# Performance work log

Hardware: AMD Instinct MI355X
Metric: run time of the kernel (lower is better)

The kernel has to match this reference:

```python
import jax, jax.numpy as jnp
import numpy as np

EMBED_DIM = 1024
HEAD_DIM = 64


def setup_inputs() -> dict:
    key = jax.random.key(0)
    ks = jax.random.split(key, 7)
    B, S = 4, 2048
    s = 1.0 / np.sqrt(EMBED_DIM)
    h = jax.random.normal(ks[0], (B, S, EMBED_DIM), dtype=jnp.float32)
    Wq = jax.random.normal(ks[1], (EMBED_DIM, HEAD_DIM), dtype=jnp.float32) * s
    bq = jax.random.normal(ks[2], (HEAD_DIM,), dtype=jnp.float32) * 0.01
    Wk = jax.random.normal(ks[3], (EMBED_DIM, HEAD_DIM), dtype=jnp.float32) * s
    bk = jax.random.normal(ks[4], (HEAD_DIM,), dtype=jnp.float32) * 0.01
    Wv = jax.random.normal(ks[5], (EMBED_DIM, HEAD_DIM), dtype=jnp.float32) * s
    bv = jax.random.normal(ks[6], (HEAD_DIM,), dtype=jnp.float32) * 0.01
    return {"h": h, "Wq": Wq, "bq": bq, "Wk": Wk, "bk": bk, "Wv": Wv, "bv": bv}


def reference(h, Wq, bq, Wk, bk, Wv, bv):
    # Linear projections: h [B,S,E] -> q,k [B,S,D]
    q = jnp.einsum("bse,ed->bsd", h, Wq) + bq
    k = jnp.einsum("bse,ed->bsd", h, Wk) + bk
    v = jnp.einsum("bse,ed->bsd", h, Wv) + bv  # computed but UNUSED (faithful to source)
    del v
    scale = 1.0 / jnp.sqrt(jnp.asarray(HEAD_DIM, dtype=q.dtype))
    # scores [B, Sq, Sk]
    scores = jnp.einsum("bqd,bkd->bqk", q, k) * scale
    # NOTE: source uses softmax over dim=1 (query axis), not the key axis
    weights = jax.nn.softmax(scores, axis=1)
    # NOTE: source passes h (not v) as the value tensor
    out = jnp.einsum("bqk,bke->bqe", weights, h)  # [B, Sq, E]
    return out
```

## Files before the change

kernel.cpp:

```cpp
#include <hip/hip_runtime.h>
#include <hip/hip_bf16.h>
#include <math.h>

#define EMBED 1024
#define HDIM  64
#define BATCH 4
#define SEQ   2048

typedef __attribute__((ext_vector_type(8))) short short8;
typedef __attribute__((ext_vector_type(4))) float f32x4;
typedef unsigned int u32;
typedef unsigned short u16;

static __device__ __forceinline__ u16 f2bf(float f) {
    union { float f; u32 u; } v; v.f = f;
    u32 r = v.u + 0x7fffu + ((v.u >> 16) & 1u);
    return (u16)(r >> 16);
}

static __device__ __forceinline__ void gload_lds16(const u16* g, u16* l) {
    __builtin_amdgcn_global_load_lds(
        (const __attribute__((address_space(1))) u32*)g,
        (__attribute__((address_space(3))) u32*)l, 16, 0, 0);
}

__global__ __launch_bounds__(256) void wt_kernel(
    const float* __restrict__ Wq, const float* __restrict__ Wk,
    u16* __restrict__ WqT, u16* __restrict__ WkT)
{
    __shared__ float tile[64][65];
    const float* W = blockIdx.y ? Wk : Wq;
    u16* WT = blockIdx.y ? WkT : WqT;
    int e0 = blockIdx.x * 64;
    int t = threadIdx.x, c = t & 63, r4 = t >> 6;
    for (int r = r4; r < 64; r += 4)
        tile[r][c] = W[(size_t)(e0 + r) * HDIM + c];
    __syncthreads();
    for (int d = r4; d < 64; d += 4)
        WT[(size_t)d * EMBED + e0 + c] = f2bf(tile[c][d]);
}

__global__ __launch_bounds__(256) void proj_kernel(
    const float* __restrict__ h, const u16* __restrict__ WqT, const u16* __restrict__ WkT,
    const float* __restrict__ bq, const float* __restrict__ bk,
    u16* __restrict__ Qbf, u16* __restrict__ Kbf)
{
    __shared__ u16 hs[2][16][136];
    int b = blockIdx.x >> 7, s0 = (blockIdx.x & 127) * 16;
    int t = threadIdx.x, lane = t & 63, w = t >> 6;
    int l15 = lane & 15, quad = lane >> 4;
    int pj = w >> 1, nh = (w & 1) * 32;
    const float* hb = h + ((size_t)b * SEQ + s0) * EMBED;
    const u16* Wp = pj ? WkT : WqT;
    int r = t >> 4, c4 = (t & 15) * 4;

    f32x4 pre0 = *(const f32x4*)(hb + (size_t)r * EMBED + c4);
    f32x4 pre1 = *(const f32x4*)(hb + (size_t)r * EMBED + 64 + c4);
    f32x4 accA[2], accB[2];
    accA[0] = accA[1] = accB[0] = accB[1] = (f32x4){0.f, 0.f, 0.f, 0.f};

    const u16* Wrow0 = Wp + (size_t)(nh + l15) * EMBED;
    const u16* Wrow1 = Wp + (size_t)(nh + 16 + l15) * EMBED;

    short8 cw[8];
#pragma unroll
    for (int i = 0; i < 4; i++) {
        cw[i]     = *(const short8*)(Wrow0 + i * 32 + quad * 8);
        cw[4 + i] = *(const short8*)(Wrow1 + i * 32 + quad * 8);
    }

    for (int it = 0; it < 8; ++it) {
        int ec = it * 128, buf = it & 1;
        uint2 pk;
        pk.x = (u32)f2bf(pre0[0]) | ((u32)f2bf(pre0[1]) << 16);
        pk.y = (u32)f2bf(pre0[2]) | ((u32)f2bf(pre0[3]) << 16);
        *(uint2*)&hs[buf][r][c4] = pk;
        pk.x = (u32)f2bf(pre1[0]) | ((u32)f2bf(pre1[1]) << 16);
        pk.y = (u32)f2bf(pre1[2]) | ((u32)f2bf(pre1[3]) << 16);
        *(uint2*)&hs[buf][r][64 + c4] = pk;
        __syncthreads();

        if (it + 1 < 8) {
            pre0 = *(const f32x4*)(hb + (size_t)r * EMBED + ec + 128 + c4);
            pre1 = *(const f32x4*)(hb + (size_t)r * EMBED + ec + 192 + c4);
        }
        short8 nw[8];
#pragma unroll
        for (int i = 0; i < 8; i++) nw[i] = cw[i];
        if (it + 1 < 8) {
#pragma unroll
            for (int i = 0; i < 4; i++) {
                nw[i]     = *(const short8*)(Wrow0 + ec + 128 + i * 32 + quad * 8);
                nw[4 + i] = *(const short8*)(Wrow1 + ec + 128 + i * 32 + quad * 8);
            }
        }

        short8 a0 = *(const short8*)&hs[buf][l15][quad * 8];
        short8 a1 = *(const short8*)&hs[buf][l15][32 + quad * 8];
        short8 a2 = *(const short8*)&hs[buf][l15][64 + quad * 8];
        short8 a3 = *(const short8*)&hs[buf][l15][96 + quad * 8];
        accA[0] = __builtin_amdgcn_mfma_f32_16x16x32_bf16(a0, cw[0], accA[0], 0, 0, 0);
        accA[1] = __builtin_amdgcn_mfma_f32_16x16x32_bf16(a0, cw[4], accA[1], 0, 0, 0);
        accB[0] = __builtin_amdgcn_mfma_f32_16x16x32_bf16(a1, cw[1], accB[0], 0, 0, 0);
        accB[1] = __builtin_amdgcn_mfma_f32_16x16x32_bf16(a1, cw[5], accB[1], 0, 0, 0);
        accA[0] = __builtin_amdgcn_mfma_f32_16x16x32_bf16(a2, cw[2], accA[0], 0, 0, 0);
        accA[1] = __builtin_amdgcn_mfma_f32_16x16x32_bf16(a2, cw[6], accA[1], 0, 0, 0);
        accB[0] = __builtin_amdgcn_mfma_f32_16x16x32_bf16(a3, cw[3], accB[0], 0, 0, 0);
        accB[1] = __builtin_amdgcn_mfma_f32_16x16x32_bf16(a3, cw[7], accB[1], 0, 0, 0);
#pragma unroll
        for (int i = 0; i < 8; i++) cw[i] = nw[i];
    }

    const float* bias = pj ? bk : bq;
    float scale = pj ? 1.0f : 0.125f;
    u16* outp = pj ? Kbf : Qbf;
    float bv0 = bias[nh + l15], bv1 = bias[nh + 16 + l15];
#pragma unroll
    for (int rr = 0; rr < 4; rr++) {
        size_t row = (size_t)b * SEQ + s0 + quad * 4 + rr;
        outp[row * HDIM + nh + l15]      = f2bf((accA[0][rr] + accB[0][rr] + bv0) * scale);
        outp[row * HDIM + nh + 16 + l15] = f2bf((accA[1][rr] + accB[1][rr] + bv1) * scale);
    }
}

__global__ __launch_bounds__(256) void sw_kernel(
    const u16* __restrict__ Qbf, const u16* __restrict__ Kbf,
    u16* __restrict__ Wmat, float* __restrict__ invl)
{
    __shared__ float sl[4][16];
    int b = blockIdx.y;
    int k0 = blockIdx.x * 16;
    int t = threadIdx.x, lane = t & 63, w = t >> 6;
    int l15 = lane & 15, quad = lane >> 4;
    const u16* Qb = Qbf + (size_t)b * SEQ * HDIM;
    const u16* Kb = Kbf + (size_t)b * SEQ * HDIM;
    u16* Wb = Wmat + (size_t)b * SEQ * SEQ;
    short8 kf0 = *(const short8*)(Kb + (size_t)(k0 + l15) * HDIM + quad * 8);
    short8 kf1 = *(const short8*)(Kb + (size_t)(k0 + l15) * HDIM + 32 + quad * 8);
    f32x4 lacc = {0.f, 0.f, 0.f, 0.f};
    int qs = w * 512;
    const u16* qpa = Qb + (size_t)(qs + l15) * HDIM;
    const u16* qpb = Qb + (size_t)(qs + 16 + l15) * HDIM;
    short8 cf0a = *(const short8*)(qpa + quad * 8);
    short8 cf1a = *(const short8*)(qpa + 32 + quad * 8);
    short8 cf0b = *(const short8*)(qpb + quad * 8);
    short8 cf1b = *(const short8*)(qpb + 32 + quad * 8);

    for (int q0 = qs; q0 < qs + 512; q0 += 32) {
        short8 nf0a = cf0a, nf1a = cf1a, nf0b = cf0b, nf1b = cf1b;
        if (q0 + 32 < qs + 512) {
            const u16* na = Qb + (size_t)(q0 + 32 + l15) * HDIM;
            const u16* nb = Qb + (size_t)(q0 + 48 + l15) * HDIM;
            nf0a = *(const short8*)(na + quad * 8);
            nf1a = *(const short8*)(na + 32 + quad * 8);
            nf0b = *(const short8*)(nb + quad * 8);
            nf1b = *(const short8*)(nb + 32 + quad * 8);
        }
        f32x4 aa = {0.f, 0.f, 0.f, 0.f}, ab = {0.f, 0.f, 0.f, 0.f};
        aa = __builtin_amdgcn_mfma_f32_16x16x32_bf16(kf0, cf0a, aa, 0, 0, 0);
        ab = __builtin_amdgcn_mfma_f32_16x16x32_bf16(kf0, cf0b, ab, 0, 0, 0);
        aa = __builtin_amdgcn_mfma_f32_16x16x32_bf16(kf1, cf1a, aa, 0, 0, 0);
        ab = __builtin_amdgcn_mfma_f32_16x16x32_bf16(kf1, cf1b, ab, 0, 0, 0);
        float e0 = __expf(aa[0]), e1 = __expf(aa[1]);
        float e2 = __expf(aa[2]), e3 = __expf(aa[3]);
        float g0 = __expf(ab[0]), g1 = __expf(ab[1]);
        float g2 = __expf(ab[2]), g3 = __expf(ab[3]);
        lacc[0] += e0 + g0; lacc[1] += e1 + g1;
        lacc[2] += e2 + g2; lacc[3] += e3 + g3;
        uint2 pa, pb;
        pa.x = (u32)f2bf(e0) | ((u32)f2bf(e1) << 16);
        pa.y = (u32)f2bf(e2) | ((u32)f2bf(e3) << 16);
        pb.x = (u32)f2bf(g0) | ((u32)f2bf(g1) << 16);
        pb.y = (u32)f2bf(g2) | ((u32)f2bf(g3) << 16);
        *(uint2*)(Wb + (size_t)(q0 + l15) * SEQ + k0 + quad * 4) = pa;
        *(uint2*)(Wb + (size_t)(q0 + 16 + l15) * SEQ + k0 + quad * 4) = pb;
        cf0a = nf0a; cf1a = nf1a; cf0b = nf0b; cf1b = nf1b;
    }
#pragma unroll
    for (int m = 1; m <= 8; m <<= 1) {
        lacc[0] += __shfl_xor(lacc[0], m, 64);
        lacc[1] += __shfl_xor(lacc[1], m, 64);
        lacc[2] += __shfl_xor(lacc[2], m, 64);
        lacc[3] += __shfl_xor(lacc[3], m, 64);
    }
    if (l15 == 0) {
        sl[w][quad * 4 + 0] = lacc[0];
        sl[w][quad * 4 + 1] = lacc[1];
        sl[w][quad * 4 + 2] = lacc[2];
        sl[w][quad * 4 + 3] = lacc[3];
    }
    __syncthreads();
    if (t < 16)
        invl[b * SEQ + k0 + t] =
            1.0f / ((sl[0][t] + sl[1][t]) + (sl[2][t] + sl[3][t]));
}

__global__ __launch_bounds__(256) void tscale_kernel(
    const float* __restrict__ h, const float* __restrict__ invl,
    u16* __restrict__ hT)
{
    __shared__ float tile[64][65];
    int b  = blockIdx.z;
    int s0 = blockIdx.x * 64, e0 = blockIdx.y * 64;
    int t = threadIdx.x, c = t & 63, r4 = t >> 6;
    const float* hb = h + (size_t)b * SEQ * EMBED;
    for (int r = r4; r < 64; r += 4)
        tile[r][c] = hb[(size_t)(s0 + r) * EMBED + e0 + c];
    __syncthreads();
    float il = invl[b * SEQ + s0 + c];
    u16* hTb = hT + (size_t)b * EMBED * SEQ;
    for (int er = r4; er < 64; er += 4)
        hTb[(size_t)(e0 + er) * SEQ + s0 + c] = f2bf(tile[c][er] * il);
}

__global__ __launch_bounds__(512, 2) void out_gemm_kernel(
    const u16* __restrict__ Wmat, const u16* __restrict__ hT, float* __restrict__ out)
{
    __shared__ u16 As[3][256 * 64];
    __shared__ u16 Bs[3][128 * 64];
    int b = blockIdx.z;
    int q0 = blockIdx.x * 256, e0 = blockIdx.y * 128;
    int t = threadIdx.x, lane = t & 63, w = t >> 6;
    int l15 = lane & 15, quad = lane >> 4;
    const u16* Wb  = Wmat + (size_t)b * SEQ * SEQ;
    const u16* hTb = hT + (size_t)b * EMBED * SEQ;
    int wm = w >> 1, wn = w & 1;
    int wq = wm * 64, we = wn * 64;

    f32x4 acc[4][4];
#pragma unroll
    for (int qi = 0; qi < 4; qi++)
#pragma unroll
        for (int ej = 0; ej < 4; ej++) acc[qi][ej] = (f32x4){0.f, 0.f, 0.f, 0.f};

    int st_rl = lane >> 3;
    int st_pc = lane & 7;

#define STAGE_A(si, k0, ld)                                                    \
    {                                                                          \
        int rowb = w * 32 + (ld) * 8;                                          \
        int row  = rowb + st_rl;                                               \
        int cg   = st_pc ^ (row & 7);                \
        gload_lds16(Wb + (size_t)(q0 + row) * SEQ + (k0) + cg * 8,             \
                    &As[si][rowb * 64] + lane * 8);                            \
    }
#define STAGE_B(si, k0, ld)                                                    \
    {                                                                          \
        int rowb = w * 16 + (ld) * 8;                                          \
        int row  = rowb + st_rl;                                               \
        int cg   = st_pc ^ (row & 7);                                          \
        gload_lds16(hTb + (size_t)(e0 + row) * SEQ + (k0) + cg * 8,            \
                    &Bs[si][rowb * 64] + lane * 8);                            \
    }

#define LDFRAGS(kf)                                                            \
    {                                                                          \
        _Pragma("unroll")                                                      \
        for (int i = 0; i < 4; i++) {                                          \
            int ra  = wq + i * 16 + l15;                                       \
            int pca = ((kf) * 4 + quad) ^ (ra & 7);                            \
            af[i] = *(const short8*)(Ab + ra * 64 + pca * 8);                  \
        }                                                                      \
        _Pragma("unroll")                                                      \
        for (int j = 0; j < 4; j++) {                                          \
            int rb  = we + j * 16 + l15;                                       \
            int pcb = ((kf) * 4 + quad) ^ (rb & 7);                            \
            bfr[j] = *(const short8*)(Bb + rb * 64 + pcb * 8);                 \
        }                                                                      \
    }

#define MFMA16                                                                 \
    {                                                                          \
        _Pragma("unroll")                                                      \
        for (int qi = 0; qi < 4; qi++)                                         \
            _Pragma("unroll")                                                  \
            for (int ej = 0; ej < 4; ej++)                                     \
                acc[qi][ej] = __builtin_amdgcn_mfma_f32_16x16x32_bf16(         \
                    af[qi], bfr[ej], acc[qi][ej], 0, 0, 0);                    \
    }

    STAGE_A(0, 0, 0) STAGE_A(0, 0, 1) STAGE_A(0, 0, 2) STAGE_A(0, 0, 3)
    STAGE_B(0, 0, 0) STAGE_B(0, 0, 1)
    STAGE_A(1, 64, 0) STAGE_A(1, 64, 1) STAGE_A(1, 64, 2) STAGE_A(1, 64, 3)
    STAGE_B(1, 64, 0) STAGE_B(1, 64, 1)
    asm volatile("s_waitcnt vmcnt(6)" ::: "memory");
    __builtin_amdgcn_s_barrier();

    for (int kt = 0; kt < 32; ++kt) {
        int s = kt % 3;
        const u16* Ab = &As[s][0];
        const u16* Bb = &Bs[s][0];
        int s2 = (kt + 2) % 3;
        int k2 = (kt + 2) * 64;
        bool st = (kt + 2) < 32;
        short8 af[4], bfr[4];

        LDFRAGS(0)
        if (st) { STAGE_A(s2, k2, 0) STAGE_A(s2, k2, 1) STAGE_B(s2, k2, 0) }
        __builtin_amdgcn_s_barrier();
        asm volatile("s_waitcnt lgkmcnt(0)" ::: "memory");
        __builtin_amdgcn_sched_barrier(0);
        __builtin_amdgcn_s_setprio(1);
        MFMA16
        __builtin_amdgcn_s_setprio(0);
        __builtin_amdgcn_s_barrier();

        LDFRAGS(1)
        if (st) { STAGE_A(s2, k2, 2) STAGE_A(s2, k2, 3) STAGE_B(s2, k2, 1) }
        __builtin_amdgcn_s_barrier();
        asm volatile("s_waitcnt lgkmcnt(0)" ::: "memory");
        __builtin_amdgcn_sched_barrier(0);
        __builtin_amdgcn_s_setprio(1);
        MFMA16
        __builtin_amdgcn_s_setprio(0);
        if (kt < 30)       { asm volatile("s_waitcnt vmcnt(6)" ::: "memory"); }
        else if (kt == 30) { asm volatile("s_waitcnt vmcnt(0)" ::: "memory"); }
        __builtin_amdgcn_s_barrier();
    }
#undef STAGE_A
#undef STAGE_B
#undef LDFRAGS
#undef MFMA16

    float* outb = out + (size_t)b * SEQ * EMBED;
#pragma unroll
    for (int qi = 0; qi < 4; qi++)
#pragma unroll
        for (int ej = 0; ej < 4; ej++)
#pragma unroll
            for (int r = 0; r < 4; r++)
                outb[(size_t)(q0 + wq + qi * 16 + quad * 4 + r) * EMBED
                     + e0 + we + ej * 16 + l15] = acc[qi][ej][r];
}

extern "C" void kernel_launch(void* const* d_in, const int* in_sizes, int n_in,
                              void* d_out, int out_size, void* d_ws, size_t ws_size,
                              hipStream_t stream) {
    (void)in_sizes; (void)n_in; (void)out_size; (void)ws_size;
    const float* h  = (const float*)d_in[0];
    const float* Wq = (const float*)d_in[1];
    const float* bq = (const float*)d_in[2];
    const float* Wk = (const float*)d_in[3];
    const float* bk = (const float*)d_in[4];
    float* out = (float*)d_out;

    char* ws = (char*)d_ws;
    u16*   Qbf  = (u16*)(ws);
    u16*   Kbf  = (u16*)(ws + (1ull << 20));
    u16*   hT   = (u16*)(ws + (2ull << 20));
    float* invl = (float*)(ws + (18ull << 20));
    u16*   WqT  = (u16*)(ws + (18ull << 20) + (128ull << 10));
    u16*   WkT  = (u16*)(ws + (18ull << 20) + (256ull << 10));
    u16*   Wmat = (u16*)(ws + (19ull << 20));

    hipLaunchKernelGGL(wt_kernel, dim3(16, 2), dim3(256), 0, stream, Wq, Wk, WqT, WkT);
    hipLaunchKernelGGL(proj_kernel, dim3(512), dim3(256), 0, stream,
                       h, WqT, WkT, bq, bk, Qbf, Kbf);
    hipLaunchKernelGGL(sw_kernel, dim3(128, 4), dim3(256), 0, stream,
                       Qbf, Kbf, Wmat, invl);
    hipLaunchKernelGGL(tscale_kernel, dim3(32, 16, 4), dim3(256), 0, stream,
                       h, invl, hT);
    hipLaunchKernelGGL(out_gemm_kernel, dim3(8, 8, 4), dim3(512), 0, stream,
                       Wmat, hT, out);
}
```

Measured before the change: 178.2 us.

## Split K across warp groups in out GEMM, vectorize transpose, deepen proj prefetch

The output GEMM now assigns each group of four warps one half of each 64-wide K slice, so every warp covers a 128x64 output tile with 8x4 accumulators. The two halves are summed through shared memory in the epilogue. This cuts per-warp B-fragment reloads and raises MFMA work per LDS read, at the cost of doubled accumulator registers, which may hurt occupancy at 2 blocks per CU. The transpose-scale kernel switches to float4 loads and packed 4-element bf16 stores. The projection kernel prefetches h two iterations ahead instead of one.

```diff
diff --git a/kernel.cpp b/kernel.cpp
--- a/kernel.cpp
+++ b/kernel.cpp
@@ -54,8 +54,10 @@
     const u16* Wp = pj ? WkT : WqT;
     int r = t >> 4, c4 = (t & 15) * 4;
 
-    f32x4 pre0 = *(const f32x4*)(hb + (size_t)r * EMBED + c4);
-    f32x4 pre1 = *(const f32x4*)(hb + (size_t)r * EMBED + 64 + c4);
+    f32x4 preA0 = *(const f32x4*)(hb + (size_t)r * EMBED + c4);
+    f32x4 preA1 = *(const f32x4*)(hb + (size_t)r * EMBED + 64 + c4);
+    f32x4 preB0 = *(const f32x4*)(hb + (size_t)r * EMBED + 128 + c4);
+    f32x4 preB1 = *(const f32x4*)(hb + (size_t)r * EMBED + 192 + c4);
     f32x4 accA[2], accB[2];
     accA[0] = accA[1] = accB[0] = accB[1] = (f32x4){0.f, 0.f, 0.f, 0.f};
 
@@ -72,17 +74,18 @@
     for (int it = 0; it < 8; ++it) {
         int ec = it * 128, buf = it & 1;
         uint2 pk;
-        pk.x = (u32)f2bf(pre0[0]) | ((u32)f2bf(pre0[1]) << 16);
-        pk.y = (u32)f2bf(pre0[2]) | ((u32)f2bf(pre0[3]) << 16);
+        pk.x = (u32)f2bf(preA0[0]) | ((u32)f2bf(preA0[1]) << 16);
+        pk.y = (u32)f2bf(preA0[2]) | ((u32)f2bf(preA0[3]) << 16);
         *(uint2*)&hs[buf][r][c4] = pk;
-        pk.x = (u32)f2bf(pre1[0]) | ((u32)f2bf(pre1[1]) << 16);
-        pk.y = (u32)f2bf(pre1[2]) | ((u32)f2bf(pre1[3]) << 16);
+        pk.x = (u32)f2bf(preA1[0]) | ((u32)f2bf(preA1[1]) << 16);
+        pk.y = (u32)f2bf(preA1[2]) | ((u32)f2bf(preA1[3]) << 16);
         *(uint2*)&hs[buf][r][64 + c4] = pk;
         __syncthreads();
 
-        if (it + 1 < 8) {
-            pre0 = *(const f32x4*)(hb + (size_t)r * EMBED + ec + 128 + c4);
-            pre1 = *(const f32x4*)(hb + (size_t)r * EMBED + ec + 192 + c4);
+        preA0 = preB0; preA1 = preB1;
+        if (it + 2 < 8) {
+            preB0 = *(const f32x4*)(hb + (size_t)r * EMBED + ec + 256 + c4);
+            preB1 = *(const f32x4*)(hb + (size_t)r * EMBED + ec + 320 + c4);
         }
         short8 nw[8];
 #pragma unroll
@@ -202,36 +205,51 @@
     __shared__ float tile[64][65];
     int b  = blockIdx.z;
     int s0 = blockIdx.x * 64, e0 = blockIdx.y * 64;
-    int t = threadIdx.x, c = t & 63, r4 = t >> 6;
+    int t = threadIdx.x;
+    int r16 = t >> 4, c4 = (t & 15) * 4;
     const float* hb = h + (size_t)b * SEQ * EMBED;
-    for (int r = r4; r < 64; r += 4)
-        tile[r][c] = hb[(size_t)(s0 + r) * EMBED + e0 + c];
+#pragma unroll
+    for (int rr = r16; rr < 64; rr += 16) {
+        f32x4 v = *(const f32x4*)(hb + (size_t)(s0 + rr) * EMBED + e0 + c4);
+        *(f32x4*)&tile[rr][c4] = v;
+    }
     __syncthreads();
-    float il = invl[b * SEQ + s0 + c];
+    f32x4 il4 = *(const f32x4*)(invl + b * SEQ + s0 + c4);
     u16* hTb = hT + (size_t)b * EMBED * SEQ;
-    for (int er = r4; er < 64; er += 4)
-        hTb[(size_t)(e0 + er) * SEQ + s0 + c] = f2bf(tile[c][er] * il);
+#pragma unroll
+    for (int er = r16; er < 64; er += 16) {
+        u16 p0 = f2bf(tile[c4 + 0][er] * il4[0]);
+        u16 p1 = f2bf(tile[c4 + 1][er] * il4[1]);
+        u16 p2 = f2bf(tile[c4 + 2][er] * il4[2]);
+        u16 p3 = f2bf(tile[c4 + 3][er] * il4[3]);
+        uint2 pk;
+        pk.x = (u32)p0 | ((u32)p1 << 16);
+        pk.y = (u32)p2 | ((u32)p3 << 16);
+        *(uint2*)(hTb + (size_t)(e0 + er) * SEQ + s0 + c4) = pk;
+    }
 }
 
 __global__ __launch_bounds__(512, 2) void out_gemm_kernel(
     const u16* __restrict__ Wmat, const u16* __restrict__ hT, float* __restrict__ out)
 {
-    __shared__ u16 As[3][256 * 64];
-    __shared__ u16 Bs[3][128 * 64];
+    __shared__ __align__(16) char smem[3 * 49152];
+#define ASLOT(si) ((u16*)(smem + (size_t)(si) * 49152))
+#define BSLOT(si) ((u16*)(smem + (size_t)(si) * 49152 + 32768))
     int b = blockIdx.z;
     int q0 = blockIdx.x * 256, e0 = blockIdx.y * 128;
     int t = threadIdx.x, lane = t & 63, w = t >> 6;
     int l15 = lane & 15, quad = lane >> 4;
     const u16* Wb  = Wmat + (size_t)b * SEQ * SEQ;
     const u16* hTb = hT + (size_t)b * EMBED * SEQ;
-    int wm = w >> 1, wn = w & 1;
-    int wq = wm * 64, we = wn * 64;
-
-    f32x4 acc[4][4];
-#pragma unroll
-    for (int qi = 0; qi < 4; qi++)
-#pragma unroll
-        for (int ej = 0; ej < 4; ej++) acc[qi][ej] = (f32x4){0.f, 0.f, 0.f, 0.f};
+    int kf = w >> 2;
+    int wm = (w >> 1) & 1, wn = w & 1;
+    int wq = wm * 128, we = wn * 64;
+
+    f32x4 acc[8][4];
+#pragma unroll
+    for (int i = 0; i < 8; i++)
+#pragma unroll
+        for (int j = 0; j < 4; j++) acc[i][j] = (f32x4){0.f, 0.f, 0.f, 0.f};
 
     int st_rl = lane >> 3;
     int st_pc = lane & 7;
@@ -242,7 +260,7 @@
         int row  = rowb + st_rl;                                               \
         int cg   = st_pc ^ (row & 7);                \
         gload_lds16(Wb + (size_t)(q0 + row) * SEQ + (k0) + cg * 8,             \
-                    &As[si][rowb * 64] + lane * 8);                            \
+                    ASLOT(si) + rowb * 64 + lane * 8);                         \
     }
 #define STAGE_B(si, k0, ld)                                                    \
     {                                                                          \
@@ -250,33 +268,36 @@
         int row  = rowb + st_rl;                                               \
         int cg   = st_pc ^ (row & 7);                                          \
         gload_lds16(hTb + (size_t)(e0 + row) * SEQ + (k0) + cg * 8,            \
-                    &Bs[si][rowb * 64] + lane * 8);                            \
-    }
-
-#define LDFRAGS(kf)                                                            \
+                    BSLOT(si) + rowb * 64 + lane * 8);                         \
+    }
+
+#define LDFRAGS_A(i0)                                                          \
     {                                                                          \
         _Pragma("unroll")                                                      \
-        for (int i = 0; i < 4; i++) {                                          \
-            int ra  = wq + i * 16 + l15;                                       \
-            int pca = ((kf) * 4 + quad) ^ (ra & 7);                            \
-            af[i] = *(const short8*)(Ab + ra * 64 + pca * 8);                  \
+        for (int ii = 0; ii < 4; ii++) {                                       \
+            int ra  = wq + ((i0) + ii) * 16 + l15;                             \
+            int pca = (kf * 4 + quad) ^ (ra & 7);                              \
+            af[ii] = *(const short8*)(Ab + ra * 64 + pca * 8);                 \
         }                                                                      \
+    }
+#define LDFRAGS_B                                                              \
+    {                                                                          \
         _Pragma("unroll")                                                      \
         for (int j = 0; j < 4; j++) {                                          \
             int rb  = we + j * 16 + l15;                                       \
-            int pcb = ((kf) * 4 + quad) ^ (rb & 7);                            \
+            int pcb = (kf * 4 + quad) ^ (rb & 7);                              \
             bfr[j] = *(const short8*)(Bb + rb * 64 + pcb * 8);                 \
         }                                                                      \
     }
 
-#define MFMA16                                                                 \
+#define MFMA16(i0)                                                             \
     {                                                                          \
         _Pragma("unroll")                                                      \
-        for (int qi = 0; qi < 4; qi++)                                         \
+        for (int ii = 0; ii < 4; ii++)                                         \
             _Pragma("unroll")                                                  \
-            for (int ej = 0; ej < 4; ej++)                                     \
-                acc[qi][ej] = __builtin_amdgcn_mfma_f32_16x16x32_bf16(         \
-                    af[qi], bfr[ej], acc[qi][ej], 0, 0, 0);                    \
+            for (int j = 0; j < 4; j++)                                        \
+                acc[(i0) + ii][j] = __builtin_amdgcn_mfma_f32_16x16x32_bf16(   \
+                    af[ii], bfr[j], acc[(i0) + ii][j], 0, 0, 0);               \
     }
 
     STAGE_A(0, 0, 0) STAGE_A(0, 0, 1) STAGE_A(0, 0, 2) STAGE_A(0, 0, 3)
@@ -288,30 +309,31 @@
 
     for (int kt = 0; kt < 32; ++kt) {
         int s = kt % 3;
-        const u16* Ab = &As[s][0];
-        const u16* Bb = &Bs[s][0];
+        const u16* Ab = ASLOT(s);
+        const u16* Bb = BSLOT(s);
         int s2 = (kt + 2) % 3;
-        int k2 = (kt + 2) * 64;
+        int k2 = (kt + 2) * 64 + kf * 0;
         bool st = (kt + 2) < 32;
         short8 af[4], bfr[4];
 
-        LDFRAGS(0)
+        LDFRAGS_A(0)
+        LDFRAGS_B
         if (st) { STAGE_A(s2, k2, 0) STAGE_A(s2, k2, 1) STAGE_B(s2, k2, 0) }
         __builtin_amdgcn_s_barrier();
         asm volatile("s_waitcnt lgkmcnt(0)" ::: "memory");
         __builtin_amdgcn_sched_barrier(0);
         __builtin_amdgcn_s_setprio(1);
-        MFMA16
+        MFMA16(0)
         __builtin_amdgcn_s_setprio(0);
         __builtin_amdgcn_s_barrier();
 
-        LDFRAGS(1)
+        LDFRAGS_A(4)
         if (st) { STAGE_A(s2, k2, 2) STAGE_A(s2, k2, 3) STAGE_B(s2, k2, 1) }
         __builtin_amdgcn_s_barrier();
         asm volatile("s_waitcnt lgkmcnt(0)" ::: "memory");
         __builtin_amdgcn_sched_barrier(0);
         __builtin_amdgcn_s_setprio(1);
-        MFMA16
+        MFMA16(4)
         __builtin_amdgcn_s_setprio(0);
         if (kt < 30)       { asm volatile("s_waitcnt vmcnt(6)" ::: "memory"); }
         else if (kt == 30) { asm volatile("s_waitcnt vmcnt(0)" ::: "memory"); }
@@ -319,18 +341,37 @@
     }
 #undef STAGE_A
 #undef STAGE_B
-#undef LDFRAGS
+#undef LDFRAGS_A
+#undef LDFRAGS_B
 #undef MFMA16
 
-    float* outb = out + (size_t)b * SEQ * EMBED;
-#pragma unroll
-    for (int qi = 0; qi < 4; qi++)
-#pragma unroll
-        for (int ej = 0; ej < 4; ej++)
-#pragma unroll
-            for (int r = 0; r < 4; r++)
-                outb[(size_t)(q0 + wq + qi * 16 + quad * 4 + r) * EMBED
-                     + e0 + we + ej * 16 + l15] = acc[qi][ej][r];
+    float* red = (float*)smem;
+    if (w >= 4) {
+        float* reg = red + (size_t)(w & 3) * 8192;
+#pragma unroll
+        for (int i = 0; i < 8; i++)
+#pragma unroll
+            for (int j = 0; j < 4; j++)
+                *(f32x4*)(reg + ((i * 4 + j) * 64 + lane) * 4) = acc[i][j];
+    }
+    __syncthreads();
+    if (w < 4) {
+        float* reg = red + (size_t)w * 8192;
+        float* outb = out + (size_t)b * SEQ * EMBED;
+#pragma unroll
+        for (int i = 0; i < 8; i++)
+#pragma unroll
+            for (int j = 0; j < 4; j++) {
+                f32x4 o = *(const f32x4*)(reg + ((i * 4 + j) * 64 + lane) * 4);
+                o += acc[i][j];
+#pragma unroll
+                for (int r = 0; r < 4; r++)
+                    outb[(size_t)(q0 + wq + i * 16 + quad * 4 + r) * EMBED
+                         + e0 + we + j * 16 + l15] = o[r];
+            }
+    }
+#undef ASLOT
+#undef BSLOT
 }
 
 extern "C" void kernel_launch(void* const* d_in, const int* in_sizes, int n_in,
```

Measured after the change: 174.0 us. 2.4% less time.
